# Kernel tuning notes

Hardware: AMD Instinct MI355X
Metric: run time of the kernel (lower is better)

## Reference

```python
import jax, jax.numpy as jnp
import numpy as np
import math

# quantum-number configuration (matches init_kwargs N=4, L=3, M=3)
N_Q, L_Q, M_Q = 4, 3, 3
OUTC, INC = 16, 16
OUTN, CONV_N = 4096, 27  # output grid points, 3x3x3 conv stencil


def _qnums(N, K, M):
    """Enumerate (n, l, m) exactly as DCConv3dKernelUnitPolynomials._Polynomial_initial."""
    lst = []
    for n in range(1, N + 1):
        for l in range(0, min(n, K + 1)):
            for m in range(-l, l + 1):
                if abs(m) <= M:
                    lst.append((n, l, m))
    return lst

QNUMS = _qnums(N_Q, L_Q, M_Q)
NUM_BASIS = len(QNUMS)  # 30


def _laguerre_coeffs(k, alpha):
    # generalized Laguerre L_k^alpha coefficients, ascending powers
    return [((-1.0) ** i) * math.comb(k + alpha, k - i) / math.factorial(i) for i in range(k + 1)]


def _horner(coeffs_ascending, x):
    acc = jnp.zeros_like(x) + coeffs_ascending[-1]
    for c in reversed(coeffs_ascending[:-1]):
        acc = acc * x + c
    return acc


def _plm(l, m, x):
    """Associated Legendre P_l^m(x) with Condon-Shortley phase, static l,m>=0."""
    somx2 = jnp.sqrt(jnp.clip(1.0 - x * x, 0.0))
    pmm = jnp.ones_like(x)
    for i in range(m):
        pmm = pmm * (-(2.0 * i + 1.0)) * somx2
    if l == m:
        return pmm
    pmmp1 = x * (2.0 * m + 1.0) * pmm
    if l == m + 1:
        return pmmp1
    for ll in range(m + 2, l + 1):
        pll = ((2.0 * ll - 1.0) * x * pmmp1 - (ll + m - 1.0) * pmm) / (ll - m)
        pmm, pmmp1 = pmmp1, pll
    return pmmp1


def _hwfr(n, l, m, r, theta, phi):
    """Real hydrogen wavefunction psi_{nlm}(r, theta, phi), Bohr radius = 1."""
    # radial part R_{nl}
    norm_r = math.sqrt((2.0 / n) ** 3 * math.factorial(n - l - 1) / (2.0 * n * math.factorial(n + l)))
    rho = (2.0 / n) * r
    R = norm_r * jnp.exp(-0.5 * rho) * (rho ** l) * _horner(_laguerre_coeffs(n - l - 1, 2 * l + 1), rho)
    # real spherical harmonic Y_{lm}
    am = abs(m)
    k_lm = math.sqrt((2.0 * l + 1.0) / (4.0 * math.pi) * math.factorial(l - am) / math.factorial(l + am))
    P = _plm(l, am, jnp.cos(theta))
    if m > 0:
        Y = math.sqrt(2.0) * k_lm * P * jnp.cos(am * phi)
    elif m < 0:
        Y = math.sqrt(2.0) * k_lm * P * jnp.sin(am * phi)
    else:
        Y = k_lm * P
    return R * Y


def _basis(position):
    # position: (OutN, conv_n, 3) -> (OutN, conv_n, B)
    r, theta, phi = position[..., 0], position[..., 1], position[..., 2]
    return jnp.stack([_hwfr(n, l, m, r, theta, phi) for (n, l, m) in QNUMS], axis=-1)


def setup_inputs() -> dict:
    key = jax.random.key(0)
    k1, k2, k3, k4 = jax.random.split(key, 4)
    r = 5.0 * jax.random.uniform(k1, (OUTN, CONV_N), dtype=jnp.float32)
    theta = jnp.pi * jax.random.uniform(k2, (OUTN, CONV_N), dtype=jnp.float32)
    phi = 2.0 * jnp.pi * jax.random.uniform(k3, (OUTN, CONV_N), dtype=jnp.float32)
    position = jnp.stack([r, theta, phi], axis=-1)  # (OutN, conv_n, 3)
    coeffs = jax.random.normal(k4, (OUTC, INC, NUM_BASIS), dtype=jnp.float32)
    return {"position": position, "coeffs": coeffs}


def reference(position, coeffs):
    # bas: (OutN, conv_n, B); coeffs: (OutC, InC, B) -> (OutC, InC, OutN, conv_n)
    bas = _basis(position)
    return jnp.einsum("xnb,oib->oixn", bas, coeffs)
```

## Files before the change

### kernel.cpp

```cpp
#include <hip/hip_runtime.h>
#include <math.h>

#define OUTN  4096
#define CONVN 27
#define NPTS  (OUTN * CONVN)
#define NPAIR (NPTS / 2)
#define NB    30
#define NOI   256
#define OI_CHUNK 32
#define NCHUNK (NOI / OI_CHUNK)

typedef float floatx2 __attribute__((ext_vector_type(2)));

__device__ __forceinline__ void eval_basis(float r, float theta, float phi,
                                           float* __restrict__ bas)
{
    const float ct = cosf(theta);
    const float st = sqrtf(fmaxf(1.0f - ct * ct, 0.0f));
    float s1, c1;
    sincosf(phi, &s1, &c1);
    const float c2 = c1 * c1 - s1 * s1;
    const float s2 = 2.0f * c1 * s1;
    const float c3 = c2 * c1 - s2 * s1;
    const float s3 = s2 * c1 + c2 * s1;

    const float P11 = -st;
    const float P20 = 0.5f * (3.0f * ct * ct - 1.0f);
    const float P21 = -3.0f * ct * st;
    const float P22 = 3.0f * (1.0f - ct * ct);
    const float P30 = 0.5f * ct * (5.0f * ct * ct - 3.0f);
    const float P31 = -1.5f * (5.0f * ct * ct - 1.0f) * st;
    const float P32 = 15.0f * ct * (1.0f - ct * ct);
    const float P33 = -15.0f * st * st * st;

    const float PI   = 3.14159265358979323846f;
    const float K00  = sqrtf(1.0f / (4.0f * PI));
    const float K10  = sqrtf(3.0f / (4.0f * PI));
    const float SK11 = sqrtf(2.0f) * sqrtf(3.0f / (8.0f * PI));
    const float K20  = sqrtf(5.0f / (4.0f * PI));
    const float SK21 = sqrtf(2.0f) * sqrtf(5.0f / (24.0f * PI));
    const float SK22 = sqrtf(2.0f) * sqrtf(5.0f / (96.0f * PI));
    const float K30  = sqrtf(7.0f / (4.0f * PI));
    const float SK31 = sqrtf(2.0f) * sqrtf(7.0f / (48.0f * PI));
    const float SK32 = sqrtf(2.0f) * sqrtf(7.0f / (480.0f * PI));
    const float SK33 = sqrtf(2.0f) * sqrtf(7.0f / (2880.0f * PI));

    const float Y00  = K00;
    const float Y1m1 = SK11 * P11 * s1;
    const float Y10  = K10 * ct;
    const float Y1p1 = SK11 * P11 * c1;
    const float Y2m2 = SK22 * P22 * s2;
    const float Y2m1 = SK21 * P21 * s1;
    const float Y20  = K20 * P20;
    const float Y2p1 = SK21 * P21 * c1;
    const float Y2p2 = SK22 * P22 * c2;
    const float Y3m3 = SK33 * P33 * s3;
    const float Y3m2 = SK32 * P32 * s2;
    const float Y3m1 = SK31 * P31 * s1;
    const float Y30  = K30 * P30;
    const float Y3p1 = SK31 * P31 * c1;
    const float Y3p2 = SK32 * P32 * c2;
    const float Y3p3 = SK33 * P33 * c3;

    const float e1 = expf(-r);
    const float e2 = expf(-0.5f * r);
    const float e3 = expf(-r * (1.0f / 3.0f));
    const float e4 = expf(-0.25f * r);
    const float q2 = r;
    const float q3 = (2.0f / 3.0f) * r;
    const float q4 = 0.5f * r;

    const float R10 = 2.0f * e1;
    const float R20 = sqrtf(1.0f / 8.0f)       * e2 * (2.0f - q2);
    const float R21 = sqrtf(1.0f / 24.0f)      * e2 * q2;
    const float R30 = sqrtf(8.0f / 486.0f)     * e3 * (3.0f - 3.0f * q3 + 0.5f * q3 * q3);
    const float R31 = sqrtf(8.0f / 3888.0f)    * e3 * q3 * (4.0f - q3);
    const float R32 = sqrtf(8.0f / 19440.0f)   * e3 * q3 * q3;
    const float R40 = 0.0625f                  * e4 * (4.0f - 6.0f * q4 + 2.0f * q4 * q4 - q4 * q4 * q4 * (1.0f / 6.0f));
    const float R41 = sqrtf(0.25f / 960.0f)    * e4 * q4 * (10.0f - 5.0f * q4 + 0.5f * q4 * q4);
    const float R42 = sqrtf(0.125f / 5760.0f)  * e4 * q4 * q4 * (6.0f - q4);
    const float R43 = sqrtf(0.125f / 40320.0f) * e4 * q4 * q4 * q4;

    bas[0]  = R10 * Y00;
    bas[1]  = R20 * Y00;
    bas[2]  = R21 * Y1m1;
    bas[3]  = R21 * Y10;
    bas[4]  = R21 * Y1p1;
    bas[5]  = R30 * Y00;
    bas[6]  = R31 * Y1m1;
    bas[7]  = R31 * Y10;
    bas[8]  = R31 * Y1p1;
    bas[9]  = R32 * Y2m2;
    bas[10] = R32 * Y2m1;
    bas[11] = R32 * Y20;
    bas[12] = R32 * Y2p1;
    bas[13] = R32 * Y2p2;
    bas[14] = R40 * Y00;
    bas[15] = R41 * Y1m1;
    bas[16] = R41 * Y10;
    bas[17] = R41 * Y1p1;
    bas[18] = R42 * Y2m2;
    bas[19] = R42 * Y2m1;
    bas[20] = R42 * Y20;
    bas[21] = R42 * Y2p1;
    bas[22] = R42 * Y2p2;
    bas[23] = R43 * Y3m3;
    bas[24] = R43 * Y3m2;
    bas[25] = R43 * Y3m1;
    bas[26] = R43 * Y30;
    bas[27] = R43 * Y3p1;
    bas[28] = R43 * Y3p2;
    bas[29] = R43 * Y3p3;
}

__global__ __launch_bounds__(256)
void dcconv_basis_gemm(const float* __restrict__ pos,
                       const float* __restrict__ coeffs,
                       float* __restrict__ out)
{
    const int pair = blockIdx.x * 256 + threadIdx.x;
    const int oi0  = blockIdx.y * OI_CHUNK;

    const floatx2* pv = reinterpret_cast<const floatx2*>(pos) + pair * 3;
    const floatx2 pv0 = pv[0];
    const floatx2 pv1 = pv[1];
    const floatx2 pv2 = pv[2];

    float basA[NB], basB[NB];
    eval_basis(pv0.x, pv0.y, pv1.x, basA);
    eval_basis(pv1.y, pv2.x, pv2.y, basB);

    floatx2 bas2[NB];
    #pragma unroll
    for (int b = 0; b < NB; ++b) {
        bas2[b].x = basA[b];
        bas2[b].y = basB[b];
    }

    floatx2* outp = reinterpret_cast<floatx2*>(out) + pair;
    #pragma unroll 4
    for (int k = 0; k < OI_CHUNK; ++k) {
        const float* cf = coeffs + (size_t)(oi0 + k) * NB;
        floatx2 acc = (floatx2)(0.0f);
        #pragma unroll
        for (int b = 0; b < NB; ++b) {
            const float c = cf[b];
            floatx2 cv; cv.x = c; cv.y = c;
            acc = __builtin_elementwise_fma(cv, bas2[b], acc);
        }
        __builtin_nontemporal_store(acc, &outp[(size_t)(oi0 + k) * (NPTS / 2)]);
    }
}

extern "C" void kernel_launch(void* const* d_in, const int* in_sizes, int n_in,
                              void* d_out, int out_size, void* d_ws, size_t ws_size,
                              hipStream_t stream) {
    const float* pos    = (const float*)d_in[0];
    const float* coeffs = (const float*)d_in[1];
    float* out = (float*)d_out;

    dim3 grid(NPAIR / 256, NCHUNK);
    dim3 block(256);
    dcconv_basis_gemm<<<grid, block, 0, stream>>>(pos, coeffs, out);
}
```

Measured before the change: 32.01 us.

## Split basis evaluation into a separate kernel writing a workspace buffer

Adds a kernel that evaluates the 30 hydrogen basis functions once per point into a workspace. A second kernel then reads them to do the coefficient contraction. This removes the repeated basis recomputation across the 8 output-channel chunks. In exchange it adds a workspace round trip of about 26 MB of traffic and an extra launch. The original fused kernel is kept as the fallback when the workspace is too small.

```diff
diff --git a/kernel.cpp b/kernel.cpp
--- a/kernel.cpp
+++ b/kernel.cpp
@@ -114,28 +114,30 @@
 }
 
 __global__ __launch_bounds__(256)
-void dcconv_basis_gemm(const float* __restrict__ pos,
-                       const float* __restrict__ coeffs,
-                       float* __restrict__ out)
+void basis_eval_kernel(const float* __restrict__ pos,
+                       float* __restrict__ bas_ws)
+{
+    const int p = blockIdx.x * 256 + threadIdx.x;
+    float bas[NB];
+    eval_basis(pos[p * 3 + 0], pos[p * 3 + 1], pos[p * 3 + 2], bas);
+    #pragma unroll
+    for (int b = 0; b < NB; ++b)
+        bas_ws[(size_t)b * NPTS + p] = bas[b];
+}
+
+__global__ __launch_bounds__(256)
+void einsum_kernel(const float* __restrict__ bas_ws,
+                   const float* __restrict__ coeffs,
+                   float* __restrict__ out)
 {
     const int pair = blockIdx.x * 256 + threadIdx.x;
     const int oi0  = blockIdx.y * OI_CHUNK;
 
-    const floatx2* pv = reinterpret_cast<const floatx2*>(pos) + pair * 3;
-    const floatx2 pv0 = pv[0];
-    const floatx2 pv1 = pv[1];
-    const floatx2 pv2 = pv[2];
-
-    float basA[NB], basB[NB];
-    eval_basis(pv0.x, pv0.y, pv1.x, basA);
-    eval_basis(pv1.y, pv2.x, pv2.y, basB);
-
+    const floatx2* wp = reinterpret_cast<const floatx2*>(bas_ws);
     floatx2 bas2[NB];
     #pragma unroll
-    for (int b = 0; b < NB; ++b) {
-        bas2[b].x = basA[b];
-        bas2[b].y = basB[b];
-    }
+    for (int b = 0; b < NB; ++b)
+        bas2[b] = wp[(size_t)b * NPAIR + pair];
 
     floatx2* outp = reinterpret_cast<floatx2*>(out) + pair;
     #pragma unroll 4
@@ -148,7 +150,41 @@
             floatx2 cv; cv.x = c; cv.y = c;
             acc = __builtin_elementwise_fma(cv, bas2[b], acc);
         }
-        __builtin_nontemporal_store(acc, &outp[(size_t)(oi0 + k) * (NPTS / 2)]);
+        __builtin_nontemporal_store(acc, &outp[(size_t)(oi0 + k) * NPAIR]);
+    }
+}
+
+__global__ __launch_bounds__(256)
+void dcconv_fused(const float* __restrict__ pos,
+                  const float* __restrict__ coeffs,
+                  float* __restrict__ out)
+{
+    const int pair = blockIdx.x * 256 + threadIdx.x;
+    const int oi0  = blockIdx.y * OI_CHUNK;
+
+    const floatx2* pv = reinterpret_cast<const floatx2*>(pos) + pair * 3;
+    const floatx2 pv0 = pv[0], pv1 = pv[1], pv2 = pv[2];
+
+    float basA[NB], basB[NB];
+    eval_basis(pv0.x, pv0.y, pv1.x, basA);
+    eval_basis(pv1.y, pv2.x, pv2.y, basB);
+
+    floatx2 bas2[NB];
+    #pragma unroll
+    for (int b = 0; b < NB; ++b) { bas2[b].x = basA[b]; bas2[b].y = basB[b]; }
+
+    floatx2* outp = reinterpret_cast<floatx2*>(out) + pair;
+    #pragma unroll 4
+    for (int k = 0; k < OI_CHUNK; ++k) {
+        const float* cf = coeffs + (size_t)(oi0 + k) * NB;
+        floatx2 acc = (floatx2)(0.0f);
+        #pragma unroll
+        for (int b = 0; b < NB; ++b) {
+            const float c = cf[b];
+            floatx2 cv; cv.x = c; cv.y = c;
+            acc = __builtin_elementwise_fma(cv, bas2[b], acc);
+        }
+        __builtin_nontemporal_store(acc, &outp[(size_t)(oi0 + k) * NPAIR]);
     }
 }
 
@@ -159,7 +195,13 @@
     const float* coeffs = (const float*)d_in[1];
     float* out = (float*)d_out;
 
-    dim3 grid(NPAIR / 256, NCHUNK);
-    dim3 block(256);
-    dcconv_basis_gemm<<<grid, block, 0, stream>>>(pos, coeffs, out);
-}
+    const size_t WS_NEEDED = (size_t)NB * NPTS * sizeof(float);
+
+    if (ws_size >= WS_NEEDED) {
+        float* bas_ws = (float*)d_ws;
+        basis_eval_kernel<<<dim3(NPTS / 256), dim3(256), 0, stream>>>(pos, bas_ws);
+        einsum_kernel<<<dim3(NPAIR / 256, NCHUNK), dim3(256), 0, stream>>>(bas_ws, coeffs, out);
+    } else {
+        dcconv_fused<<<dim3(NPAIR / 256, NCHUNK), dim3(256), 0, stream>>>(pos, coeffs, out);
+    }
+}
```

Result: slower. 40.65 us (+27.0%).
